# Kernel optimization log

Hardware: AMD Instinct MI355X
Metric: run time of the kernel (lower is better)

Reference implementation:

```python
import jax, jax.numpy as jnp
import numpy as np

THRESHOLD = 0.0
NEG_SLOPE = 0.2   # DGL GATConv leaky_relu negative slope
N, EMB, C = 4096, 2048, 10


def _gat(x, W, a_l, a_r, logm):
    """Dense masked DGL-style GATConv. x:[N,in], W:[in,H*D], a_l/a_r:[H,D],
    logm:[N,N] log edge-multiplicity (-inf where no edge). Returns [N,H,D]."""
    H, D = a_l.shape
    feat = (x @ W).reshape(-1, H, D)                      # [N,H,D]
    el = jnp.einsum('nhd,hd->nh', feat, a_l)              # per-src score
    er = jnp.einsum('nhd,hd->nh', feat, a_r)              # per-dst score
    e = jax.nn.leaky_relu(el[:, None, :] + er[None, :, :], NEG_SLOPE)  # [src,dst,H]
    logits = e + logm[:, :, None]                          # mask + self-loop multiplicity
    alpha = jax.nn.softmax(logits, axis=0)                 # edge softmax over incoming src per dst
    return jnp.einsum('sdh,she->dhe', alpha, feat)         # [N,H,D]


def setup_inputs() -> dict:
    key = jax.random.key(0)
    ks = jax.random.split(key, 12)
    s = lambda fan_in: 1.0 / np.sqrt(fan_in)
    return {
        'deep_features': jax.random.normal(ks[0], (N, EMB), jnp.float32),
        'W1':  jax.random.normal(ks[1], (2048, 1024), jnp.float32) * s(2048),
        'al1': jax.random.normal(ks[2], (1, 1024), jnp.float32) * s(1024),
        'ar1': jax.random.normal(ks[3], (1, 1024), jnp.float32) * s(1024),
        'W2':  jax.random.normal(ks[4], (1024, 2 * 512), jnp.float32) * s(1024),
        'al2': jax.random.normal(ks[5], (2, 512), jnp.float32) * s(512),
        'ar2': jax.random.normal(ks[6], (2, 512), jnp.float32) * s(512),
        'lin1_w': jax.random.normal(ks[7], (2048 + 512, 1024), jnp.float32) * s(2560),
        'lin1_b': jnp.zeros((1024,), jnp.float32),
        'c1_w': jax.random.normal(ks[8], (1024, C), jnp.float32) * s(1024),
        'c1_b': jnp.zeros((C,), jnp.float32),
        'c2_w': jax.random.normal(ks[9], (2048, C), jnp.float32) * s(2048),
        'c2_b': jnp.zeros((C,), jnp.float32),
    }


def reference(deep_features, W1, al1, ar1, W2, al2, ar2,
              lin1_w, lin1_b, c1_w, c1_b, c2_w, c2_b):
    df = deep_features                                     # [N,2048] (ResNet50 features)
    # --- build_graph: cosine similarity threshold graph on detached features ---
    dfs = jax.lax.stop_gradient(df)
    znorm = jnp.linalg.norm(dfs, axis=1, keepdims=True)
    sim = (dfs @ dfs.T) / (znorm @ znorm.T)                # symmetric cosine similarity
    n = df.shape[0]
    # adjacency from threshold (includes self since sim_ii=1>thr) + extra self-loop from dgl.add_self_loop
    mult = (sim > THRESHOLD).astype(df.dtype) + jnp.eye(n, dtype=df.dtype)
    logm = jnp.where(mult > 0, jnp.log(jnp.maximum(mult, 1e-12)), -jnp.inf)
    # --- GAT stack ---
    x = jax.nn.relu(_gat(df, W1, al1, ar1, logm).reshape(n, 1024))
    x = _gat(x, W2, al2, ar2, logm).sum(axis=1)            # sum over 2 heads -> [N,512]
    x = jnp.concatenate([df, x], axis=1)                   # [N,2560]
    x = jax.nn.leaky_relu(x @ lin1_w + lin1_b, 0.01)       # F.leaky_relu default slope
    logits1 = x @ c1_w + c1_b
    logits2 = df @ c2_w + c2_b
    return logits1, logits2
```

## Files before the change

### kernel.cpp

```cpp
#include <hip/hip_runtime.h>
#include <hip/hip_bf16.h>

typedef __hip_bfloat16 bf16;
typedef __attribute__((ext_vector_type(8))) short short8;
typedef __attribute__((ext_vector_type(4))) float f32x4;

#define NN 4096
#define L2E 1.4426950408889634f

__device__ inline float br_sum(float v, float* sd){
  #pragma unroll
  for(int s=32; s>0; s>>=1) v += __shfl_down(v, s, 64);
  int t = threadIdx.x;
  if ((t & 63) == 0) sd[t >> 6] = v;
  __syncthreads();
  float r = (sd[0] + sd[1]) + (sd[2] + sd[3]);
  __syncthreads();
  return r;
}

__device__ inline void gl2lds(const bf16* g, unsigned int* lds){
  __builtin_amdgcn_global_load_lds(
      (const __attribute__((address_space(1))) unsigned int*)g,
      (__attribute__((address_space(3))) unsigned int*)lds, 16, 0, 0);
}

template<int N> __device__ inline void waitvm(){
  if constexpr (N==0)       asm volatile("s_waitcnt vmcnt(0)" ::: "memory");
  else if constexpr (N==4)  asm volatile("s_waitcnt vmcnt(4)" ::: "memory");
  else if constexpr (N==6)  asm volatile("s_waitcnt vmcnt(6)" ::: "memory");
  else if constexpr (N==8)  asm volatile("s_waitcnt vmcnt(8)" ::: "memory");
  else if constexpr (N==12) asm volatile("s_waitcnt vmcnt(12)" ::: "memory");
  else if constexpr (N==18) asm volatile("s_waitcnt vmcnt(18)" ::: "memory");
  else if constexpr (N==24) asm volatile("s_waitcnt vmcnt(24)" ::: "memory");
}
__device__ inline void pipe_barrier(){
  __builtin_amdgcn_s_barrier();
  asm volatile("" ::: "memory");
}

__global__ __launch_bounds__(256)
void prep_all_k(const float* __restrict__ df, const float* __restrict__ W1,
                const float* __restrict__ W2, const float* __restrict__ lw,
                bf16* __restrict__ dfb, bf16* __restrict__ W1tb,
                bf16* __restrict__ W2tb, bf16* __restrict__ lwcat,
                const float* __restrict__ c2w, const float* __restrict__ c2b,
                float* __restrict__ out2)
{
  int b = blockIdx.x, t = threadIdx.x;
  if (b < 8192){
    int i = (b*256 + t)*4;
    f32x4 v = *(const f32x4*)(df + i);
    #pragma unroll
    for(int q=0;q<4;q++) dfb[i+q] = __float2bfloat16(v[q]);
    return;
  }
  if (b >= 9600){
    __shared__ float sd4[4];
    int n = b - 9600;
    float acc[10] = {};
    for(int k=t; k<2048; k+=256){
      float xv = df[(size_t)n*2048 + k];
      #pragma unroll
      for(int c=0;c<10;c++) acc[c] += xv * c2w[k*10 + c];
    }
    #pragma unroll
    for(int c=0;c<10;c++){
      float r = br_sum(acc[c], sd4);
      if(t==0) out2[n*10 + c] = r + c2b[c];
    }
    return;
  }
  b -= 8192;
  const float* src; bf16* dst; int rb, cb, dstld; bool dup=false;
  if (b < 512){            src=W1; dst=W1tb;  rb=(b>>4)<<6; cb=(b&15)<<6; dstld=2048; }
  else if (b < 768){ b-=512; src=W2; dst=W2tb; rb=(b>>4)<<6; cb=(b&15)<<6; dstld=1024; }
  else { b-=768; src=lw; dst=lwcat; rb=(b>>4)<<6; cb=(b&15)<<6; dstld=3072; dup=(rb>=2048); }
  __shared__ bf16 tile[64][65];
  #pragma unroll
  for(int i=0;i<16;i++){
    int lin=i*256+t, tr=lin>>6, tc=lin&63;
    tile[tr][tc] = __float2bfloat16(src[(size_t)(rb+tr)*1024 + cb+tc]);
  }
  __syncthreads();
  #pragma unroll
  for(int i=0;i<16;i++){
    int lin=i*256+t, tc=lin>>6, tr=lin&63;
    bf16 v = tile[tr][tc];
    dst[(size_t)(cb+tc)*dstld + rb+tr] = v;
    if(dup) dst[(size_t)(cb+tc)*dstld + rb+tr + 512] = v;
  }
}

__device__ __forceinline__
void adj_body(const bf16* __restrict__ A, unsigned int* __restrict__ Cm,
              unsigned int* SH, int idx)
{
  unsigned int* As = SH;
  unsigned int* Bs = SH + 6144;
  const int tid = threadIdx.x;
  int by = (int)((65.0f - sqrtf(4225.0f - 8.0f*(float)idx)) * 0.5f);
  while ((by+1)*(65-(by+1))/2 <= idx) by++;
  while (by*(65-by)/2 > idx) by--;
  int bx = by + (idx - by*(65-by)/2);
  const int bm = by*128, bn = bx*128;
  const int lane = tid&63, wid = tid>>6;
  const int wr = (wid>>1)*64, wc = (wid&1)*64;
  const int quad = lane>>4, mr = lane&15;
  const int L4 = lane>>2;
  const int lsw = (lane&3) ^ ((lane>>3)&3);
  const int qsw4 = ((quad ^ ((mr>>1)&3)) << 2);

  f32x4 acc[4][4];
  #pragma unroll
  for(int i=0;i<4;i++)
    #pragma unroll
    for(int j=0;j<4;j++) acc[i][j] = (f32x4){0.f,0.f,0.f,0.f};

  auto stage = [&](int kb, int p){
    #pragma unroll
    for(int c2=0; c2<2; c2++){
      int row = (wid*2+c2)*16 + L4;
      gl2lds(A + (size_t)(bm+row)*2048 + kb + lsw*8, &As[p*2048 + (wid*2+c2)*256]);
      gl2lds(A + (size_t)(bn+row)*2048 + kb + lsw*8, &Bs[p*2048 + (wid*2+c2)*256]);
    }
  };
  auto compute = [&](int p){
    short8 af[4], bfr[4];
    #pragma unroll
    for(int i=0;i<4;i++)  af[i]  = *(const short8*)&As[p*2048 + (wr + i*16 + mr)*16 + qsw4];
    #pragma unroll
    for(int j=0;j<4;j++)  bfr[j] = *(const short8*)&Bs[p*2048 + (wc + j*16 + mr)*16 + qsw4];
    #pragma unroll
    for(int i=0;i<4;i++)
      #pragma unroll
      for(int j=0;j<4;j++)
        acc[i][j] = __builtin_amdgcn_mfma_f32_16x16x32_bf16(af[i], bfr[j], acc[i][j], 0,0,0);
  };

  stage(0,0); stage(32,1);
  int p = 0;
  #pragma unroll 1
  for(int it=0; it<63; it++){
    waitvm<4>();
    pipe_barrier();
    if (it+2 < 64) stage(32*(it+2), p==0?2:p-1);
    compute(p);
    p = (p==2)?0:p+1;
  }
  waitvm<0>();
  pipe_barrier();
  compute(p);

  #pragma unroll
  for(int i=0;i<4;i++){
    #pragma unroll
    for(int j=0;j<4;j++){
      int cbase = bn + wc + j*16;
      unsigned long long b[4];
      #pragma unroll
      for(int reg=0; reg<4; reg++){
        float v = acc[i][j][reg];
        unsigned long long msk = __ballot(v > 0.f);
        b[reg] = msk;
        if (mr == 0){
          int r = bm + wr + i*16 + quad*4 + reg;
          unsigned int x = (unsigned int)(msk >> (quad*16)) & 0xFFFFu;
          x = (x | (x << 8)) & 0x00FF00FFu;
          x = (x | (x << 4)) & 0x0F0F0F0Fu;
          x = (x | (x << 2)) & 0x33333333u;
          x = (x | (x << 1)) & 0x55555555u;
          if (r >= cbase && r < cbase + 16) x += 1u << (2*(r - cbase));
          Cm[(size_t)r*256 + (cbase>>4)] = x;
        }
      }
      if (bx > by){
        unsigned int x = 0;
        #pragma unroll
        for(int reg=0; reg<4; reg++){
          unsigned long long t = (b[reg] >> mr) & 0x0001000100010001ULL;
          unsigned int f = (unsigned int)((t | (t>>15) | (t>>30) | (t>>45)) & 0xFULL);
          x |= ((f&1u) | ((f&2u)<<7) | ((f&4u)<<14) | ((f&8u)<<21)) << (2*reg);
        }
        if (quad == 0){
          int c = cbase + mr;
          Cm[(size_t)c*256 + ((bm + wr + i*16)>>4)] = x;
        }
      }
    }
  }
}

template<int EPI, int TN, int DUALA, int K, int LDA, int LDBT, int LDC,
         int K1, int LDA2, int WT, int NS>
__device__ __forceinline__
void gemm_body(const bf16* __restrict__ Ag, const bf16* __restrict__ Bt,
               void* __restrict__ Cv, const float* __restrict__ bias,
               const bf16* __restrict__ Ag2, bf16* __restrict__ Ct,
               unsigned int* SH, int bid)
{
  constexpr int NJ  = TN/32;
  constexpr int D   = 2 + TN/64;
  constexpr int NIT = K/32;
  unsigned int* As = SH;
  unsigned int* Bs = SH + NS*2048;
  const int tid = threadIdx.x;
  const int by = 4*(bid&7) + ((bid>>3)&3);
  const int bx = bid>>5;
  const int bm = by*128, bn = bx*TN;
  const int lane = tid&63, wid = tid>>6;
  const int wr = (wid>>1)*64, wc = (wid&1)*(TN/2);
  const int quad = lane>>4, mr = lane&15;
  const int L4 = lane>>2;
  const int lsw = (lane&3) ^ ((lane>>3)&3);
  const int qsw4 = ((quad ^ ((mr>>1)&3)) << 2);

  f32x4 acc[4][NJ];
  #pragma unroll
  for(int i=0;i<4;i++)
    #pragma unroll
    for(int j=0;j<NJ;j++) acc[i][j] = (f32x4){0.f,0.f,0.f,0.f};

  auto stage = [&](int kb, int p){
    #pragma unroll
    for(int c2=0; c2<2; c2++){
      int row = (wid*2+c2)*16 + L4;
      const bf16* ap;
      if (DUALA && kb >= K1) ap = Ag2 + (size_t)(bm+row)*LDA2 + (kb-K1);
      else                   ap = Ag  + (size_t)(bm+row)*LDA  + kb;
      gl2lds(ap + lsw*8, &As[p*2048 + (wid*2+c2)*256]);
    }
    #pragma unroll
    for(int c2=0; c2<TN/64; c2++){
      int row = (wid*(TN/64)+c2)*16 + L4;
      gl2lds(Bt + (size_t)(bn+row)*LDBT + kb + lsw*8,
             &Bs[p*(TN*16) + (wid*(TN/64)+c2)*256]);
    }
  };
  auto compute = [&](int p){
    short8 af[4], bfr[NJ];
    #pragma unroll
    for(int i=0;i<4;i++)
      af[i]  = *(const short8*)&As[p*2048 + (wr + i*16 + mr)*16 + qsw4];
    #pragma unroll
    for(int j=0;j<NJ;j++)
      bfr[j] = *(const short8*)&Bs[p*(TN*16) + (wc + j*16 + mr)*16 + qsw4];
    #pragma unroll
    for(int i=0;i<4;i++)
      #pragma unroll
      for(int j=0;j<NJ;j++)
        acc[i][j] = __builtin_amdgcn_mfma_f32_16x16x32_bf16(af[i], bfr[j], acc[i][j], 0,0,0);
  };

  #pragma unroll
  for(int s=0; s<NS-1; s++) stage(32*s, s);
  int p = 0;
  #pragma unroll 1
  for(int it=0; it<NIT-(NS-1); it++){
    waitvm<(NS-2)*D>();
    pipe_barrier();
    stage(32*(it+NS-1), (p+NS-1)&(NS-1));
    compute(p); p=(p+1)&(NS-1);
  }
  waitvm<0>(); pipe_barrier();
  #pragma unroll 1
  for(int r=0; r<NS-1; r++){ compute(p); p=(p+1)&(NS-1); }

  #pragma unroll
  for(int i=0;i<4;i++){
    #pragma unroll
    for(int j=0;j<NJ;j++){
      #pragma unroll
      for(int reg=0; reg<4; reg++){
        int r = bm + wr + i*16 + quad*4 + reg;
        int c = bn + wc + j*16 + mr;
        float v = acc[i][j][reg];
        if (EPI==1){ ((bf16*)Cv)[(size_t)r*LDC + c] = __float2bfloat16(fmaxf(v,0.f)); }
        if (EPI==2){ ((bf16*)Cv)[(size_t)r*LDC + c] = __float2bfloat16(v); }
        if (EPI==4){ float w = v + bias[c];
                     ((float*)Cv)[(size_t)r*LDC + c] = w > 0.f ? w : 0.01f*w; }
      }
    }
  }

  if (WT){
    __syncthreads();
    bf16* T = (bf16*)SH;
    #pragma unroll
    for(int i=0;i<4;i++)
      #pragma unroll
      for(int j=0;j<NJ;j++)
        #pragma unroll
        for(int reg=0; reg<4; reg++){
          int rl = wr + i*16 + quad*4 + reg;
          int cl = wc + j*16 + mr;
          T[rl*66 + cl] = __float2bfloat16(acc[i][j][reg]);
        }
    __syncthreads();
    #pragma unroll
    for(int w=0; w<16; w++){
      int cl = wid*16 + w;
      unsigned int v = (unsigned int)(*(unsigned short*)&T[(2*lane)*66 + cl]) |
                       ((unsigned int)(*(unsigned short*)&T[(2*lane+1)*66 + cl]) << 16);
      *(unsigned int*)&Ct[(size_t)(bn+cl)*4096 + bm + 2*lane] = v;
    }
  }
}

template<int EPI, int TN, int DUALA, int K, int LDA, int LDBT, int LDC,
         int K1, int LDA2, int WT, int NS>
__global__ __launch_bounds__(256)
void gemm_k(const bf16* __restrict__ Ag, const bf16* __restrict__ Bt,
            void* __restrict__ Cv, const float* __restrict__ bias,
            const bf16* __restrict__ Ag2, bf16* __restrict__ Ct)
{
  __shared__ unsigned int SH[NS*2048 + NS*TN*16];
  gemm_body<EPI,TN,DUALA,K,LDA,LDBT,LDC,K1,LDA2,WT,NS>(
      Ag, Bt, Cv, bias, Ag2, Ct, SH, blockIdx.x);
}

__global__ __launch_bounds__(256)
void adjfeat_k(const bf16* __restrict__ dfb, unsigned int* __restrict__ mult2,
               const bf16* __restrict__ W1tb, bf16* __restrict__ featb,
               bf16* __restrict__ featT)
{
  __shared__ unsigned int SH[12288];
  int b = blockIdx.x;
  if (b < 528){
    int bs = (b&7)*66 + (b>>3);
    adj_body(dfb, mult2, SH, bs);
  } else {
    gemm_body<2,64,0,2048,2048,2048,1024,0,0,1,4>(
        dfb, W1tb, featb, nullptr, nullptr, featT, SH, b-528);
  }
}

__global__ __launch_bounds__(256)
void elr_k(const bf16* __restrict__ feat, const float* __restrict__ al,
           const float* __restrict__ ar, float* __restrict__ el,
           float* __restrict__ er, int H)
{
  __shared__ float sd[256];
  int n = blockIdx.x, t = threadIdx.x, k0 = t*4;
  float accl = 0.f, accr = 0.f;
  #pragma unroll
  for(int q=0;q<4;q++){
    float f = __bfloat162float(feat[(size_t)n*1024 + k0 + q]);
    accl += f * al[k0+q]; accr += f * ar[k0+q];
  }
  int myh = (H==2) ? (k0 >> 9) : 0;
  for(int h=0; h<H; h++){
    float rl = br_sum(myh==h ? accl : 0.f, sd);
    float rr = br_sum(myh==h ? accr : 0.f, sd);
    if(t==0){ el[h*NN+n] = rl*L2E; er[h*NN+n] = rr*L2E; }
  }
}

__global__ __launch_bounds__(256)
void colp_k(const float* __restrict__ el, const float* __restrict__ er,
            const unsigned int* __restrict__ mult2,
            float* __restrict__ cm, float* __restrict__ cinv,
            bf16* __restrict__ P)
{
  __shared__ float sd[256];
  int d = blockIdx.x & 4095, hs = blockIdx.x >> 12, t = threadIdx.x;
  el += hs*NN; er += hs*NN; cm += hs*NN; cinv += hs*NN;
  float erd = er[d];
  unsigned int bits = mult2[(size_t)d*256 + t];
  float tv[16];
  float mx = -1e30f;
  const float* ep = el + t*16;
  #pragma unroll
  for(int h=0; h<4; h++){
    f32x4 ev = *(const f32x4*)(ep + h*4);
    #pragma unroll
    for(int q2=0;q2<4;q2++){
      int q = h*4 + q2;
      unsigned int mu = (bits >> (2*q)) & 3u;
      float x = ev[q2] + erd;
      x = fmaxf(x, 0.2f*x);
      if (mu == 2u) x += 1.0f;
      tv[q] = mu ? x : -1e30f;
      mx = fmaxf(mx, tv[q]);
    }
  }
  #pragma unroll
  for(int s=32; s>0; s>>=1) mx = fmaxf(mx, __shfl_down(mx, s, 64));
  if ((t & 63) == 0) sd[t >> 6] = mx;
  __syncthreads();
  float M = fmaxf(fmaxf(sd[0], sd[1]), fmaxf(sd[2], sd[3]));
  __syncthreads();
  float sum = 0.f;
  #pragma unroll
  for(int q=0;q<16;q++) sum += (tv[q] > -1e29f) ? __builtin_exp2f(tv[q]-M) : 0.f;
  sum = br_sum(sum, sd);
  if(t==0){ cm[d] = M; cinv[d] = 1.f/sum; }
  if (hs == 0 && P){
    float inv = 1.f/sum;
    unsigned int pk[8];
    #pragma unroll
    for(int h=0; h<4; h++){
      #pragma unroll
      for(int q2=0; q2<4; q2++){
        int q = h*4+q2;
        float v = (tv[q] > -1e29f) ? __builtin_exp2f(tv[q]-M)*inv : 0.f;
        bf16 hb = __float2bfloat16(v);
        unsigned short us = *(unsigned short*)&hb;
        if (q2 & 1) pk[h*2 + (q2>>1)] |= ((unsigned int)us << 16);
        else        pk[h*2 + (q2>>1)]  = (unsigned int)us;
      }
    }
    uint4* dst = (uint4*)(P + (size_t)d*4096 + t*16);
    dst[0] = *(uint4*)&pk[0];
    dst[1] = *(uint4*)&pk[4];
  }
}

__global__ __launch_bounds__(256)
void pbuild_k(const float* __restrict__ el, const float* __restrict__ er,
              const float* __restrict__ cm, const float* __restrict__ cinv,
              const unsigned int* __restrict__ mult2, bf16* __restrict__ P)
{
  int d = blockIdx.x, t = threadIdx.x;
  const float erd = er[d], md = cm[d], invd = cinv[d];
  unsigned int bits = mult2[(size_t)d*256 + t];
  unsigned int pk[8];
  const float* ep = el + t*16;
  #pragma unroll
  for(int h=0; h<4; h++){
    f32x4 ev = *(const f32x4*)(ep + h*4);
    #pragma unroll
    for(int q2=0; q2<4; q2++){
      int q = h*4+q2;
      unsigned int mu = (bits >> (2*q)) & 3u;
      float x = ev[q2] + erd;
      x = fmaxf(x, 0.2f*x);
      float v = __builtin_exp2f(x + (mu>1u ? 1.0f : 0.0f) - md) * invd;
      v = mu ? v : 0.0f;
      bf16 hb = __float2bfloat16(v);
      unsigned short us = *(unsigned short*)&hb;
      if (q2 & 1) pk[h*2 + (q2>>1)] |= ((unsigned int)us << 16);
      else        pk[h*2 + (q2>>1)]  = (unsigned int)us;
    }
  }
  uint4* dst = (uint4*)(P + (size_t)d*4096 + t*16);
  dst[0] = *(uint4*)&pk[0];
  dst[1] = *(uint4*)&pk[4];
}

__global__ __launch_bounds__(256)
void cls2_k(const float* __restrict__ x3, const float* __restrict__ c1w,
            const float* __restrict__ c1b, float* __restrict__ out)
{
  __shared__ float sd[256];
  int n = blockIdx.x, t = threadIdx.x;
  float acc[10] = {};
  for(int k=t; k<1024; k+=256){
    float xv = x3[(size_t)n*1024 + k];
    #pragma unroll
    for(int c=0;c<10;c++) acc[c] += xv * c1w[k*10 + c];
  }
  for(int c=0;c<10;c++){
    float r = br_sum(acc[c], sd);
    if(t==0) out[n*10 + c] = r + c1b[c];
  }
}

extern "C" void kernel_launch(void* const* d_in, const int* in_sizes, int n_in,
                              void* d_out, int out_size, void* d_ws, size_t ws_size,
                              hipStream_t stream) {
  (void)in_sizes; (void)n_in; (void)out_size; (void)ws_size;
  const float* df  = (const float*)d_in[0];
  const float* W1  = (const float*)d_in[1];
  const float* al1 = (const float*)d_in[2];
  const float* ar1 = (const float*)d_in[3];
  const float* W2  = (const float*)d_in[4];
  const float* al2 = (const float*)d_in[5];
  const float* ar2 = (const float*)d_in[6];
  const float* lw  = (const float*)d_in[7];
  const float* lb  = (const float*)d_in[8];
  const float* c1w = (const float*)d_in[9];
  const float* c1b = (const float*)d_in[10];
  const float* c2w = (const float*)d_in[11];
  const float* c2b = (const float*)d_in[12];
  float* out = (float*)d_out;

  char* Wp = (char*)d_ws;
  bf16* W1tb  = (bf16*)(Wp);
  float* S    = (float*)(Wp);
  bf16* W2tb  = (bf16*)(Wp + ( 4u<<20));
  bf16* lwcat = (bf16*)(Wp + ( 6u<<20));
  unsigned int* mult2 = (unsigned int*)(Wp + (12u<<20));
  bf16* dfb   = (bf16*)(Wp + (16u<<20));
  bf16* featb = (bf16*)(Wp + (32u<<20));
  float* x3   = (float*)(Wp + (32u<<20));
  bf16* featT = (bf16*)(Wp + (40u<<20));
  bf16* x1b   = (bf16*)(Wp + (48u<<20));
  bf16* x2cat = (bf16*)(Wp + (48u<<20));
  bf16* P     = (bf16*)(Wp + (56u<<20));
  float *el1=S, *er1=S+4096, *el2=S+8192, *er2=S+16384;
  float *m1=S+24576, *i1=S+28672, *m2=S+32768, *i2=S+40960;

  prep_all_k<<<13696,256,0,stream>>>(df, W1, W2, lw, dfb, W1tb, W2tb, lwcat,
                                     c2w, c2b, out + NN*10);

  adjfeat_k<<<1040,256,0,stream>>>(dfb, mult2, W1tb, featb, featT);

  elr_k<<<NN,256,0,stream>>>(featb, al1, ar1, el1, er1, 1);
  colp_k<<<4096,256,0,stream>>>(el1, er1, mult2, m1, i1, P);

  gemm_k<1,128,0,4096,4096,4096,1024,0,0,0,4><<<256,256,0,stream>>>(
      P, featT, x1b, nullptr, nullptr, nullptr);

  gemm_k<2,64,0,1024,1024,1024,1024,0,0,1,4><<<512,256,0,stream>>>(
      x1b, W2tb, featb, nullptr, nullptr, featT);

  elr_k<<<NN,256,0,stream>>>(featb, al2, ar2, el2, er2, 2);
  colp_k<<<8192,256,0,stream>>>(el2, er2, mult2, m2, i2, P);

  gemm_k<2,64,0,4096,4096,4096,1024,0,0,0,8><<<256,256,0,stream>>>(
      P, featT, x2cat, nullptr, nullptr, nullptr);

  pbuild_k<<<4096,256,0,stream>>>(el2+NN, er2+NN, m2+NN, i2+NN, mult2, P);
  gemm_k<2,64,0,4096,4096,4096,1024,0,0,0,8><<<256,256,0,stream>>>(
      P, featT + (size_t)512*4096, x2cat + 512, nullptr, nullptr, nullptr);

  gemm_k<4,128,1,3072,2048,3072,1024,2048,1024,0,4><<<256,256,0,stream>>>(
      dfb, lwcat, x3, lb, x2cat, nullptr);

  cls2_k<<<4096,256,0,stream>>>(x3, c1w, c1b, out);
}
```

Before: 478.0 us.

## Build both layer-2 head probability matrices at once and aggregate in one launch

When the workspace is large enough, the layer-2 column-softmax kernel writes the probability matrices for both heads into separate buffers. A single 512-block aggregation kernel then computes both heads' outputs concurrently. This replaces the sequence of gemm, pbuild and gemm, which ran two half-filled launches and rebuilt the second matrix. The layer-1 aggregation gemm's pipeline-stage parameter goes from 4 to 8, and the adjacency block swizzle is dropped. The cost is an extra 32MB P2 buffer, and the agg2 kernel uses 4 stages instead of 8.

```diff
diff --git a/kernel.cpp b/kernel.cpp
--- a/kernel.cpp
+++ b/kernel.cpp
@@ -320,6 +320,19 @@
 }
 
 __global__ __launch_bounds__(256)
+void agg2_k(const bf16* __restrict__ P, const bf16* __restrict__ P2,
+            const bf16* __restrict__ featT, bf16* __restrict__ x2cat)
+{
+  __shared__ unsigned int SH[4*2048 + 4*64*16];
+  int b = blockIdx.x;
+  const bf16* A = (b < 256) ? P : P2;
+  const bf16* B = (b < 256) ? featT : featT + (size_t)512*4096;
+  bf16* C = (b < 256) ? x2cat : x2cat + 512;
+  gemm_body<2,64,0,4096,4096,4096,1024,0,0,0,4>(
+      A, B, C, nullptr, nullptr, nullptr, SH, b & 255);
+}
+
+__global__ __launch_bounds__(256)
 void adjfeat_k(const bf16* __restrict__ dfb, unsigned int* __restrict__ mult2,
                const bf16* __restrict__ W1tb, bf16* __restrict__ featb,
                bf16* __restrict__ featT)
@@ -327,8 +340,7 @@
   __shared__ unsigned int SH[12288];
   int b = blockIdx.x;
   if (b < 528){
-    int bs = (b&7)*66 + (b>>3);
-    adj_body(dfb, mult2, SH, bs);
+    adj_body(dfb, mult2, SH, b);
   } else {
     gemm_body<2,64,0,2048,2048,2048,1024,0,0,1,4>(
         dfb, W1tb, featb, nullptr, nullptr, featT, SH, b-528);
@@ -360,7 +372,7 @@
 void colp_k(const float* __restrict__ el, const float* __restrict__ er,
             const unsigned int* __restrict__ mult2,
             float* __restrict__ cm, float* __restrict__ cinv,
-            bf16* __restrict__ P)
+            bf16* __restrict__ P, bf16* __restrict__ P2)
 {
   __shared__ float sd[256];
   int d = blockIdx.x & 4095, hs = blockIdx.x >> 12, t = threadIdx.x;
@@ -395,7 +407,8 @@
   for(int q=0;q<16;q++) sum += (tv[q] > -1e29f) ? __builtin_exp2f(tv[q]-M) : 0.f;
   sum = br_sum(sum, sd);
   if(t==0){ cm[d] = M; cinv[d] = 1.f/sum; }
-  if (hs == 0 && P){
+  bf16* Pd = (hs == 0) ? P : P2;
+  if (Pd){
     float inv = 1.f/sum;
     unsigned int pk[8];
     #pragma unroll
@@ -410,7 +423,7 @@
         else        pk[h*2 + (q2>>1)]  = (unsigned int)us;
       }
     }
-    uint4* dst = (uint4*)(P + (size_t)d*4096 + t*16);
+    uint4* dst = (uint4*)(Pd + (size_t)d*4096 + t*16);
     dst[0] = *(uint4*)&pk[0];
     dst[1] = *(uint4*)&pk[4];
   }
@@ -469,7 +482,7 @@
 extern "C" void kernel_launch(void* const* d_in, const int* in_sizes, int n_in,
                               void* d_out, int out_size, void* d_ws, size_t ws_size,
                               hipStream_t stream) {
-  (void)in_sizes; (void)n_in; (void)out_size; (void)ws_size;
+  (void)in_sizes; (void)n_in; (void)out_size;
   const float* df  = (const float*)d_in[0];
   const float* W1  = (const float*)d_in[1];
   const float* al1 = (const float*)d_in[2];
@@ -498,6 +511,8 @@
   bf16* x1b   = (bf16*)(Wp + (48u<<20));
   bf16* x2cat = (bf16*)(Wp + (48u<<20));
   bf16* P     = (bf16*)(Wp + (56u<<20));
+  bf16* P2    = (bf16*)(Wp + (88u<<20));
+  const bool bigws = ws_size >= ((size_t)120 << 20);
   float *el1=S, *er1=S+4096, *el2=S+8192, *er2=S+16384;
   float *m1=S+24576, *i1=S+28672, *m2=S+32768, *i2=S+40960;
 
@@ -507,23 +522,26 @@
   adjfeat_k<<<1040,256,0,stream>>>(dfb, mult2, W1tb, featb, featT);
 
   elr_k<<<NN,256,0,stream>>>(featb, al1, ar1, el1, er1, 1);
-  colp_k<<<4096,256,0,stream>>>(el1, er1, mult2, m1, i1, P);
-
-  gemm_k<1,128,0,4096,4096,4096,1024,0,0,0,4><<<256,256,0,stream>>>(
+  colp_k<<<4096,256,0,stream>>>(el1, er1, mult2, m1, i1, P, nullptr);
+
+  gemm_k<1,128,0,4096,4096,4096,1024,0,0,0,8><<<256,256,0,stream>>>(
       P, featT, x1b, nullptr, nullptr, nullptr);
 
   gemm_k<2,64,0,1024,1024,1024,1024,0,0,1,4><<<512,256,0,stream>>>(
       x1b, W2tb, featb, nullptr, nullptr, featT);
 
   elr_k<<<NN,256,0,stream>>>(featb, al2, ar2, el2, er2, 2);
-  colp_k<<<8192,256,0,stream>>>(el2, er2, mult2, m2, i2, P);
-
-  gemm_k<2,64,0,4096,4096,4096,1024,0,0,0,8><<<256,256,0,stream>>>(
-      P, featT, x2cat, nullptr, nullptr, nullptr);
-
-  pbuild_k<<<4096,256,0,stream>>>(el2+NN, er2+NN, m2+NN, i2+NN, mult2, P);
-  gemm_k<2,64,0,4096,4096,4096,1024,0,0,0,8><<<256,256,0,stream>>>(
-      P, featT + (size_t)512*4096, x2cat + 512, nullptr, nullptr, nullptr);
+  colp_k<<<8192,256,0,stream>>>(el2, er2, mult2, m2, i2, P, bigws ? P2 : nullptr);
+
+  if (bigws){
+    agg2_k<<<512,256,0,stream>>>(P, P2, featT, x2cat);
+  } else {
+    gemm_k<2,64,0,4096,4096,4096,1024,0,0,0,8><<<256,256,0,stream>>>(
+        P, featT, x2cat, nullptr, nullptr, nullptr);
+    pbuild_k<<<4096,256,0,stream>>>(el2+NN, er2+NN, m2+NN, i2+NN, mult2, P);
+    gemm_k<2,64,0,4096,4096,4096,1024,0,0,0,8><<<256,256,0,stream>>>(
+        P, featT + (size_t)512*4096, x2cat + 512, nullptr, nullptr, nullptr);
+  }
 
   gemm_k<4,128,1,3072,2048,3072,1024,2048,1024,0,4><<<256,256,0,stream>>>(
       dfb, lwcat, x3, lb, x2cat, nullptr);
```

Result: faster. 445.6 us (-6.8%).
